# Kernel optimization log

Hardware: AMD Instinct MI355X
Metric: run time of the kernel (lower is better)

The kernel has to match this reference:

```python
import jax, jax.numpy as jnp
import numpy as np
import math


def _interp_linear(x, t_out):
    # x: [B, D, Lin] -> [B, D, t_out]; matches torch F.interpolate(mode='linear', align_corners=False)
    lin = x.shape[-1]
    pos = (jnp.arange(t_out, dtype=jnp.float32) + 0.5) * (lin / t_out) - 0.5
    pos = jnp.clip(pos, 0.0, lin - 1.0)
    lo = jnp.floor(pos).astype(jnp.int32)
    hi = jnp.minimum(lo + 1, lin - 1)
    w = pos - lo.astype(jnp.float32)
    return x[..., lo] * (1.0 - w) + x[..., hi] * w


def _forward(x, in_w, in_b, gq_w, gq_b, gk_w, gk_b, gv_w, gv_b, go_w, go_b, curv,
             wav0, wav1, wav2, wav3, wrec_w, wrec_b,
             te1_w, te1_b, te2_w, te2_b, td1_w, td1_b, td2_w, td2_b, bd_w, bd_b,
             cc_w, cc_b, ln_g, ln_b, mm1_w, mm1_b, mm2_w, mm2_b,
             dn1_w, dn1_b, dn2_w, dn2_b, dn3_w, dn3_b, out_w, out_b,
             noise_sched, noise):
    B, T, _ = x.shape
    L, H = curv.shape
    D = in_w.shape[1]
    hd = D // H
    dn = ('NCH', 'OIH', 'NCH')
    h = x @ in_w + in_b
    total_loss = jnp.float32(0.0)
    wavs = [wav0, wav1, wav2, wav3]
    for l in range(L):  # static small layer loop
        # ---- GeometricAttention (vectorized hyperbolic-distance softmax) ----
        q = (h @ gq_w[l] + gq_b[l]).reshape(B, T, H, hd)
        k = (h @ gk_w[l] + gk_b[l]).reshape(B, T, H, hd)
        v = (h @ gv_w[l] + gv_b[l]).reshape(B, T, H, hd)
        c = jnp.abs(curv[l]) + 1e-8                       # [H]
        cb = c[None, :, None, None]
        qn = jnp.einsum('bthd,bthd->bht', q, q)           # [B,H,T]
        kn = jnp.einsum('bthd,bthd->bht', k, k)
        qk = jnp.einsum('bihd,bjhd->bhij', q, k)          # [B,H,T,T]
        d2 = jnp.maximum(qn[:, :, :, None] + kn[:, :, None, :] - 2.0 * qk, 0.0)
        denom = jnp.maximum((1.0 - cb * qn[:, :, :, None]) * (1.0 - cb * kn[:, :, None, :]), 1e-5)
        arg = jnp.maximum(1.0 + cb * (2.0 * d2) / denom, 1.00001)
        dist = jnp.arccosh(arg) / jnp.sqrt(cb)
        attn = jax.nn.softmax(-dist, axis=-1)             # temperature = 1.0
        geom = jnp.einsum('bhij,bjhd->bihd', attn, v).reshape(B, T, D) @ go_w[l] + go_b[l]
        # ---- WaveletTransform ----
        xf = h.transpose(0, 2, 1)                          # [B,D,T]
        decomps = []
        for i, wv in enumerate(wavs):
            filt = jax.nn.softmax(wv[l], axis=-1)          # [D,K]
            K = filt.shape[-1]
            dec = jax.lax.conv_general_dilated(xf, filt[:, None, :], (1,), [(K - 1, 0)],
                                               feature_group_count=D, dimension_numbers=dn)
            dec = dec[:, :, ::2 ** (i + 1)]
            decomps.append(_interp_linear(dec, T))
        comb = jnp.concatenate(decomps, axis=1).transpose(0, 2, 1)  # [B,T,4D]
        wave = comb @ wrec_w[l] + wrec_b[l]
        # ---- TopologicalLayer ----
        tf = jax.nn.relu(h @ te1_w[l] + te1_b[l]) @ te2_w[l] + te2_b[l]
        topo = h + (jax.nn.relu(tf @ td1_w[l] + td1_b[l]) @ td2_w[l] + td2_b[l])
        bd = tf @ bd_w[l] + bd_b[l]
        total_loss = total_loss + jnp.mean(jax.nn.relu(bd[..., 0] - bd[..., 1] + 0.1))
        # ---- CausalConvolution (kernel 3, dilation 2**l) ----
        dil = 2 ** l
        pad = 2 * dil
        cc = jax.lax.conv_general_dilated(h.transpose(0, 2, 1), cc_w[l], (1,), [(pad, 0)],
                                          rhs_dilation=(dil,), dimension_numbers=dn)
        cc = (cc + cc_b[l][None, :, None]).transpose(0, 2, 1)
        # ---- combine + LayerNorm (dropout is identity in eval) ----
        s = geom + wave + topo + cc
        mu = jnp.mean(s, axis=-1, keepdims=True)
        var = jnp.var(s, axis=-1, keepdims=True)
        h = (s - mu) / jnp.sqrt(var + 1e-5) * ln_g + ln_b
    # ---- manifold mixer (T > 1 branch) ----
    last = h[:, -1]
    pen = h[:, -2]
    mix = jnp.tanh(jnp.concatenate([last, pen], axis=-1) @ mm1_w + mm1_b) @ mm2_w + mm2_b
    cur = last + mix
    # ---- diffusion refinement ----
    half = D // 2
    emb_f = jnp.exp(jnp.arange(half, dtype=jnp.float32) * (-math.log(10000.0) / (half - 1)))
    S = noise.shape[0]
    for t in range(S):  # static diffusion_steps=10
        noisy = cur + noise[t] * noise_sched[t]
        te = jnp.full((B, 1), float(t), dtype=jnp.float32) * emb_f[None, :]
        temb = jnp.concatenate([jnp.sin(te), jnp.cos(te)], axis=-1)  # [B,D]
        di = jnp.concatenate([noisy, temb], axis=-1)
        npred = jax.nn.silu(jax.nn.silu(di @ dn1_w + dn1_b) @ dn2_w + dn2_b) @ dn3_w + dn3_b
        cur = cur - npred * noise_sched[t]
    pred = cur @ out_w + out_b
    return pred, total_loss


def setup_inputs() -> dict:
    key = jax.random.key(0)
    B, T, Din, D, L, H, P, S = 16, 256, 384, 512, 6, 8, 64, 10
    ctr = [0]
    def rn(shape, s=0.05):
        ctr[0] += 1
        return jax.random.normal(jax.random.fold_in(key, ctr[0]), shape, jnp.float32) * s
    d = {}
    d['x'] = rn((B, T, Din), 1.0)
    d['in_w'] = rn((Din, D)); d['in_b'] = rn((D,), 0.01)
    for nm in ['gq', 'gk', 'gv', 'go']:
        d[nm + '_w'] = rn((L, D, D)); d[nm + '_b'] = rn((L, D), 0.01)
    d['curv'] = rn((L, H), 1.0)
    for i in range(4):
        d['wav%d' % i] = rn((L, D, 2 ** (i + 2)), 1.0)
    d['wrec_w'] = rn((L, 4 * D, D)); d['wrec_b'] = rn((L, D), 0.01)
    d['te1_w'] = rn((L, D, P)); d['te1_b'] = rn((L, P), 0.01)
    d['te2_w'] = rn((L, P, P)); d['te2_b'] = rn((L, P), 0.01)
    d['td1_w'] = rn((L, P, D)); d['td1_b'] = rn((L, D), 0.01)
    d['td2_w'] = rn((L, D, D)); d['td2_b'] = rn((L, D), 0.01)
    d['bd_w'] = rn((L, P, 2)); d['bd_b'] = rn((L, 2), 0.01)
    d['cc_w'] = rn((L, D, D, 3)); d['cc_b'] = rn((L, D), 0.01)
    d['ln_g'] = jnp.ones((D,), jnp.float32); d['ln_b'] = jnp.zeros((D,), jnp.float32)
    d['mm1_w'] = rn((2 * D, D)); d['mm1_b'] = rn((D,), 0.01)
    d['mm2_w'] = rn((D, D)); d['mm2_b'] = rn((D,), 0.01)
    d['dn1_w'] = rn((2 * D, D)); d['dn1_b'] = rn((D,), 0.01)
    d['dn2_w'] = rn((D, D)); d['dn2_b'] = rn((D,), 0.01)
    d['dn3_w'] = rn((D, D)); d['dn3_b'] = rn((D,), 0.01)
    d['out_w'] = rn((D, Din)); d['out_b'] = rn((Din,), 0.01)
    d['noise_sched'] = jnp.linspace(0.1, 0.9, S).astype(jnp.float32)
    d['noise'] = rn((S, B, D), 1.0)
    return d


def reference(x, in_w, in_b, gq_w, gq_b, gk_w, gk_b, gv_w, gv_b, go_w, go_b, curv,
              wav0, wav1, wav2, wav3, wrec_w, wrec_b,
              te1_w, te1_b, te2_w, te2_b, td1_w, td1_b, td2_w, td2_b, bd_w, bd_b,
              cc_w, cc_b, ln_g, ln_b, mm1_w, mm1_b, mm2_w, mm2_b,
              dn1_w, dn1_b, dn2_w, dn2_b, dn3_w, dn3_b, out_w, out_b,
              noise_sched, noise):
    return _forward(x, in_w, in_b, gq_w, gq_b, gk_w, gk_b, gv_w, gv_b, go_w, go_b, curv,
                    wav0, wav1, wav2, wav3, wrec_w, wrec_b,
                    te1_w, te1_b, te2_w, te2_b, td1_w, td1_b, td2_w, td2_b, bd_w, bd_b,
                    cc_w, cc_b, ln_g, ln_b, mm1_w, mm1_b, mm2_w, mm2_b,
                    dn1_w, dn1_b, dn2_w, dn2_b, dn3_w, dn3_b, out_w, out_b,
                    noise_sched, noise)
```

## Files before the change

### kernel.cpp

```cpp
#include <hip/hip_runtime.h>
#include <hip/hip_bf16.h>
#include <math.h>

#define BB 16
#define TT 256
#define DIN 384
#define DD 512
#define LL 6
#define HH 8
#define PP 64
#define SS 10
#define BT (BB*TT)

enum { ACT_NONE=0, ACT_RELU=1, ACT_TANH=2, ACT_SILU=3, ACT_RELU_TAIL=4 };

typedef __attribute__((ext_vector_type(8))) short bf16x8;
typedef __attribute__((ext_vector_type(4))) float f32x4;
typedef __hip_bfloat16 bh16;

typedef const __attribute__((address_space(1))) void gvoid_t;
typedef __attribute__((address_space(3))) void lvoid_t;
__device__ __forceinline__ void gload16(const void* g, void* l) {
    __builtin_amdgcn_global_load_lds((gvoid_t*)g, (lvoid_t*)l, 16, 0, 0);
}
// ... 412 lines not shown
                float dist = logf(arg + sqrtf((arg - 1.f) * (arg + 1.f))) * isc;
                float lg = -dist;
                acc[fm][fn][r] = lg;
                rmax[fm][r] = fmaxf(rmax[fm][r], lg);
            }
    #pragma unroll
    for (int off = 1; off < 16; off <<= 1)
        #pragma unroll
        for (int fm = 0; fm < 2; ++fm)
            #pragma unroll
            for (int r = 0; r < 4; ++r)
                rmax[fm][r] = fmaxf(rmax[fm][r], __shfl_xor(rmax[fm][r], off));
    if ((lane & 15) == 0)
        #pragma unroll
        for (int fm = 0; fm < 2; ++fm)
            #pragma unroll
            for (int r = 0; r < 4; ++r)
                redA[wn][wm*32 + fm*16 + (lane>>4)*4 + r] = rmax[fm][r];
    __syncthreads();
    #pragma unroll
    for (int fm = 0; fm < 2; ++fm)
        #pragma unroll
        for (int r = 0; r < 4; ++r)
            rmax[fm][r] = fmaxf(rmax[fm][r], redA[wn ^ 1][wm*32 + fm*16 + (lane>>4)*4 + r]);
    float rsum[2][4];
    #pragma unroll
    for (int fm = 0; fm < 2; ++fm)
        #pragma unroll
        for (int r = 0; r < 4; ++r) rsum[fm][r] = 0.f;
    #pragma unroll
    for (int fm = 0; fm < 2; ++fm)
        #pragma unroll
        for (int fn = 0; fn < 8; ++fn)
            #pragma unroll
            for (int r = 0; r < 4; ++r) {
                float e = expf(acc[fm][fn][r] - rmax[fm][r]);
                acc[fm][fn][r] = e;
                rsum[fm][r] += e;
            }
    #pragma unroll
    for (int off = 1; off < 16; off <<= 1)
        #pragma unroll
        for (int fm = 0; fm < 2; ++fm)
            #pragma unroll
            for (int r = 0; r < 4; ++r)
                rsum[fm][r] += __shfl_xor(rsum[fm][r], off);
    if ((lane & 15) == 0)
        #pragma unroll
        for (int fm = 0; fm < 2; ++fm)
            #pragma unroll
            for (int r = 0; r < 4; ++r)
                redB[wn][wm*32 + fm*16 + (lane>>4)*4 + r] = rsum[fm][r];
    __syncthreads();
    float pinv[2][4];
    #pragma unroll
    for (int fm = 0; fm < 2; ++fm)
        #pragma unroll
        for (int r = 0; r < 4; ++r)
            pinv[fm][r] = 1.f / (rsum[fm][r] + redB[wn ^ 1][wm*32 + fm*16 + (lane>>4)*4 + r]);

    f32x4 acc2[2][2];
    #pragma unroll
    for (int i = 0; i < 2; ++i)
        #pragma unroll
        for (int j = 0; j < 2; ++j) acc2[i][j] = (f32x4){0.f,0.f,0.f,0.f};

    const bh16* vbase = qkv + 1024 + hh * 64;
    for (int kt = 0; kt < 4; ++kt) {
        __syncthreads();
        if (wn == (kt >> 1)) {
            int fnb = (kt & 1) * 4;
            #pragma unroll
            for (int fm = 0; fm < 2; ++fm)
                #pragma unroll
                for (int fnl = 0; fnl < 4; ++fnl)
                    #pragma unroll
                    for (int r = 0; r < 4; ++r) {
                        int rowl = wm*32 + fm*16 + (lane>>4)*4 + r;
                        int kl = fnl*16 + (lane & 15);
                        float p = acc[fm][fnb + fnl][r] * pinv[fm][r];
                        Ps[(rowl*8 + ((kl >> 3) ^ (rowl & 7)))*8 + (kl & 7)] = __float2bfloat16(p);
                    }
        }
        #pragma unroll
        for (int j = 0; j < 2; ++j) {
            int c = threadIdx.x + j*256;
            int tr = c >> 3, chk = c & 7;
            bf16x8 v = *(const bf16x8*)(vbase + (size_t)(b*256 + kt*64 + tr)*1600 + chk*8);
            *(bf16x8*)(&Vst[tr*72 + chk*8]) = v;
        }
        __syncthreads();
        #pragma unroll
        for (int j = 0; j < 2; ++j) {
            int c = threadIdx.x + j*256;
            int col = c & 63, chk = c >> 6;
            bf16x8 v;
            #pragma unroll
            for (int e = 0; e < 8; ++e)
                v[e] = (short)Vst[(chk*8 + e)*72 + col];
            Bv[col*8 + (chk ^ (col & 7))] = v;
        }
        __syncthreads();

        bf16x8 pa[2][2], vb[2][2];
        #pragma unroll
        for (int fm = 0; fm < 2; ++fm) {
            int row = wm*32 + fm*16 + (lane & 15);
            #pragma unroll
            for (int ks = 0; ks < 2; ++ks)
                pa[fm][ks] = ((bf16x8*)Ps)[row*8 + ((ks*4 + (lane>>4)) ^ (row & 7))];
        }
        #pragma unroll
        for (int fn = 0; fn < 2; ++fn) {
            int col = wn*32 + fn*16 + (lane & 15);
            #pragma unroll
            for (int ks = 0; ks < 2; ++ks)
                vb[fn][ks] = Bv[col*8 + ((ks*4 + (lane>>4)) ^ (col & 7))];
        }
        #pragma unroll
        for (int ks = 0; ks < 2; ++ks)
            #pragma unroll
            for (int fm = 0; fm < 2; ++fm)
                #pragma unroll
                for (int fn = 0; fn < 2; ++fn)
                    acc2[fm][fn] = __builtin_amdgcn_mfma_f32_16x16x32_bf16(
                        pa[fm][ks], vb[fn][ks], acc2[fm][fn], 0, 0, 0);
    }

    #pragma unroll
    for (int fm = 0; fm < 2; ++fm)
        #pragma unroll
        for (int fn = 0; fn < 2; ++fn)
            #pragma unroll
            for (int r = 0; r < 4; ++r) {
                int rowl = wm*32 + fm*16 + (lane>>4)*4 + r;
                int col = wn*32 + fn*16 + (lane & 15);
                gmb[((size_t)(b*256 + rh*64 + rowl))*512 + hh*64 + col] =
                    __float2bfloat16(acc2[fm][fn][r]);
            }
}

__global__ __launch_bounds__(256) void fgemm_kernel(
    const bh16* __restrict__ A0, const bh16* __restrict__ A1,
    const bh16* __restrict__ A2, const bh16* __restrict__ A3,
    const bh16* __restrict__ B0, const bh16* __restrict__ B1,
    const bh16* __restrict__ B2, const bh16* __restrict__ B3,
    const float* __restrict__ bias,
    float* __restrict__ Cf0, float* __restrict__ Cf1,
    float* __restrict__ Cf2, float* __restrict__ Cf3,
    int dil, const bh16* __restrict__ zp)
{
    __shared__ bf16x8 As[128*8];
    __shared__ bf16x8 Bs[64*8];

    int bx = blockIdx.x, by = blockIdx.y;
    xcd_swizzle_always(bx, by);
    const int zz = blockIdx.z;
    const int ktlo = zz * 18;
    const int kthi = ktlo + 18;

    const int tid  = threadIdx.x;
    const int lane = tid & 63, w = tid >> 6;
    const int wm = w >> 1, wn = w & 1;
    const int row0 = by * 128, col0 = bx * 64;

    f32x4 acc[4][2];
    #pragma unroll
    for (int i = 0; i < 4; ++i)
        #pragma unroll
        for (int j = 0; j < 2; ++j) acc[i][j] = (f32x4){0.f,0.f,0.f,0.f};

    for (int kt = ktlo; kt < kthi; ++kt) {
        const bh16* Aseg; const bh16* Bseg;
        int ldas, ldbs, k0, mask_sh, addr_sh;
        if (kt < 8) {
            Aseg = A0; Bseg = B0; ldas = 512; ldbs = 512;
            k0 = kt << 6; mask_sh = 0; addr_sh = 0;
        } else if (kt < 40) {
            Aseg = A1; Bseg = B1; ldas = 2048; ldbs = 2048;
            k0 = (kt - 8) << 6; mask_sh = 0; addr_sh = 0;
        } else if (kt < 48) {
            Aseg = A2; Bseg = B2; ldas = 512; ldbs = 512;
            k0 = (kt - 40) << 6; mask_sh = 0; addr_sh = 0;
        } else {
            int kl = kt - 48, tap = kl >> 3;
            Aseg = A3; Bseg = B3; ldas = 512; ldbs = 1536;
            k0 = kl << 6;
            mask_sh = (2 - tap) * dil;
            addr_sh = mask_sh + tap;
        }
        #pragma unroll
        for (int j = 0; j < 4; ++j) {
            int c = ((w*4 + j) << 6) + lane;
            int row = c >> 3, chk = c & 7;
            int schk = chk ^ (row & 7);
            int grow = row0 + row;
            const bh16* src = ((grow & 255) >= mask_sh)
                ? (Aseg + (size_t)(grow - addr_sh)*ldas + k0 + schk*8) : zp;
            gload16(src, &As[(w*4 + j) * 64]);
        }
        #pragma unroll
        for (int j = 0; j < 2; ++j) {
            int c = ((w*2 + j) << 6) + lane;
            int row = c >> 3, chk = c & 7;
            int schk = chk ^ (row & 7);
            int gcol = col0 + row;
            gload16(Bseg + (size_t)gcol*ldbs + k0 + schk*8, &Bs[(w*2 + j) * 64]);
        }
        asm volatile("s_waitcnt vmcnt(0)" ::: "memory");
        __syncthreads();

        bf16x8 a[4][2], b[2][2];
        #pragma unroll
        for (int fm = 0; fm < 4; ++fm) {
            int row = wm*64 + fm*16 + (lane & 15);
            #pragma unroll
            for (int ks = 0; ks < 2; ++ks)
                a[fm][ks] = As[row*8 + ((ks*4 + (lane>>4)) ^ (row & 7))];
        }
        #pragma unroll
        for (int fn = 0; fn < 2; ++fn) {
            int col = wn*32 + fn*16 + (lane & 15);
            #pragma unroll
            for (int ks = 0; ks < 2; ++ks)
                b[fn][ks] = Bs[col*8 + ((ks*4 + (lane>>4)) ^ (col & 7))];
        }
        #pragma unroll
        for (int ks = 0; ks < 2; ++ks)
            #pragma unroll
            for (int fm = 0; fm < 4; ++fm)
                #pragma unroll
                for (int fn = 0; fn < 2; ++fn)
                    acc[fm][fn] = __builtin_amdgcn_mfma_f32_16x16x32_bf16(
                        a[fm][ks], b[fn][ks], acc[fm][fn], 0, 0, 0);
        __syncthreads();
    }

    float* Cf = (zz == 0) ? Cf0 : (zz == 1) ? Cf1 : (zz == 2) ? Cf2 : Cf3;
    #pragma unroll
    for (int fm = 0; fm < 4; ++fm) {
        #pragma unroll
        for (int fn = 0; fn < 2; ++fn) {
            int gc = col0 + wn*32 + fn*16 + (lane & 15);
            float bs = (zz == 0) ? bias[gc] : 0.f;
            #pragma unroll
            for (int r = 0; r < 4; ++r) {
                int gr = row0 + wm*64 + fm*16 + (lane>>4)*4 + r;
                Cf[(size_t)gr*512 + gc] = acc[fm][fn][r] + bs;
            }
        }
    }
}

__global__ __launch_bounds__(256) void hgemm16_kernel(
    const bh16* __restrict__ A, int lda, long aZ,
    const bh16* __restrict__ Bt, int ldb,
    const float* __restrict__ bias,
    const float* __restrict__ pre,
    float* __restrict__ Of, bh16* __restrict__ Ob, long oZ,
    int N, int K, int act,
    float* __restrict__ curf, bh16* __restrict__ curb,
    const float* __restrict__ scaleptr)
{
    const int z = blockIdx.z;
    A += (long)z * aZ;
    const int lane = threadIdx.x & 63, w = threadIdx.x >> 6;
    const int col0 = blockIdx.x * 64 + w * 16;
    const int ar = lane & 15;
    const int koff = (lane >> 4) * 8;
    const bh16* arow = A + (size_t)ar * lda + koff;
    const bh16* brow = Bt + (size_t)(col0 + ar) * ldb + koff;
    f32x4 acc = {0.f, 0.f, 0.f, 0.f};
    const int nkt = K >> 5;
    for (int kt0 = 0; kt0 < nkt; kt0 += 8) {
        bf16x8 av[8], bv[8];
        #pragma unroll
        for (int j = 0; j < 8; ++j) {
            av[j] = *(const bf16x8*)(arow + (size_t)(kt0 + j) * 32);
            bv[j] = *(const bf16x8*)(brow + (size_t)(kt0 + j) * 32);
        }
        #pragma unroll
        for (int j = 0; j < 8; ++j)
            acc = __builtin_amdgcn_mfma_f32_16x16x32_bf16(av[j], bv[j], acc, 0, 0, 0);
    }
    const int col = col0 + ar;
    float bs = bias ? bias[col] : 0.f;
    float sc = scaleptr ? *scaleptr : 0.f;
    #pragma unroll
    for (int r = 0; r < 4; ++r) {
        int row = (lane >> 4) * 4 + r;
        float v = acc[r] + bs;
        if (pre) v += pre[(size_t)row * N + col];
        if (act == ACT_SILU)      v = v / (1.f + expf(-v));
        else if (act == ACT_TANH) v = tanhf(v);
        if (curf) {
            size_t o = (size_t)row * 512 + col;
            float nc = curf[o] - v * sc;
            curf[o] = nc;
            curb[o] = __float2bfloat16(nc);
        } else {
            size_t o = (size_t)z * oZ + (size_t)row * N + col;
            if (Of) Of[o] = v;
            if (Ob) Ob[o] = __float2bfloat16(v);
        }
    }
}

__global__ __launch_bounds__(256) void wave4_kernel(const bh16* __restrict__ hb,
                                                    const float* __restrict__ wav0,
                                                    const float* __restrict__ wav1,
                                                    const float* __restrict__ wav2,
                                                    const float* __restrict__ wav3,
                                                    int l,
                                                    bh16* __restrict__ comb)
{
    __shared__ float dtile[66 * 64];
    __shared__ float ftile[32 * 64];
    const int dblk = blockIdx.x;
    const int iy = blockIdx.y;
    const int b = blockIdx.z;
    const int i = iy >> 1, thalf = iy & 1;
    const int Karr[4] = {4, 8, 16, 32};
    const int K = Karr[i], sv = 2 << i, Ti = 128 >> i;
    const int tid = threadIdx.x;
    const int dbase = dblk * 64;
    if (tid < 64) {
        const float* wsrc = (i == 0) ? wav0 : (i == 1) ? wav1 : (i == 2) ? wav2 : wav3;
        const float* row = wsrc + ((size_t)l * DD + dbase + tid) * K;
        float mx = -1e30f;
        for (int k = 0; k < K; ++k) mx = fmaxf(mx, row[k]);
        float s = 0.f;
        for (int k = 0; k < K; ++k) { float e = expf(row[k] - mx); ftile[k*64 + tid] = e; s += e; }
        float inv = 1.f / s;
        for (int k = 0; k < K; ++k) ftile[k*64 + tid] *= inv;
    }
    const float invsv = 1.f / (float)sv;
    const int t0 = thalf * 128;
    float p0 = ((float)t0 + 0.5f) * invsv - 0.5f;
    p0 = fminf(fmaxf(p0, 0.f), (float)(Ti - 1));
    const int jbase = (int)p0;
    float p1 = ((float)(t0 + 127) + 0.5f) * invsv - 0.5f;
    p1 = fminf(fmaxf(p1, 0.f), (float)(Ti - 1));
    const int him = min((int)p1 + 1, Ti - 1);
    const int jcount = him - jbase + 1;
    __syncthreads();
    const bh16* hcol = hb + (size_t)b * (TT * DD) + dbase;
    for (int e = tid; e < jcount * 64; e += 256) {
        int jl = e >> 6, d0 = e & 63;
        int j = jbase + jl;
        int tb = j * sv - (K - 1);
        float acc = 0.f;
        #pragma unroll 4
        for (int k = 0; k < K; ++k) {
            int t = tb + k;
            if (t >= 0)
                acc += b2f(*(const unsigned short*)(hcol + (size_t)t * DD + d0)) * ftile[k * 64 + d0];
        }
        dtile[jl * 64 + d0] = acc;
    }
    __syncthreads();
    for (int e = tid; e < 128 * 64; e += 256) {
        int tl = e >> 6, d0 = e & 63;
        int t = t0 + tl;
        float pos = ((float)t + 0.5f) * invsv - 0.5f;
        pos = fminf(fmaxf(pos, 0.f), (float)(Ti - 1));
        int lo = (int)pos;
        int hi = min(lo + 1, Ti - 1);
        float w = pos - (float)lo;
        float v = dtile[(lo - jbase) * 64 + d0] * (1.f - w) + dtile[(hi - jbase) * 64 + d0] * w;
        comb[((size_t)b * TT + t) * 2048 + i * 512 + dbase + d0] = __float2bfloat16(v);
    }
}

__global__ __launch_bounds__(256) void add_ln_kernel(const float* __restrict__ s0, const float* __restrict__ s1,
                                                     const float* __restrict__ s2, const float* __restrict__ s3,
                                                     float* __restrict__ h, bh16* __restrict__ hb,
                                                     const float* __restrict__ g, const float* __restrict__ be)
{
    int lane = threadIdx.x & 63, wid = threadIdx.x >> 6;
    size_t row = (size_t)blockIdx.x * 4 + wid;
    const float* sr0 = s0 + row * DD;
    const float* sr1 = s1 + row * DD;
    const float* sr2 = s2 + row * DD;
    const float* sr3 = s3 + row * DD;
    float* hr = h + row * DD;
    bh16* hbr = hb + row * DD;
    float xv[8]; float sum = 0.f;
    #pragma unroll
    for (int u = 0; u < 8; ++u) {
        int c = lane + u * 64;
        xv[u] = sr0[c] + sr1[c] + sr2[c] + sr3[c] + hr[c];
        sum += xv[u];
    }
    #pragma unroll
    for (int off = 32; off; off >>= 1) sum += __shfl_xor(sum, off);
    float mu = sum * (1.f / 512.f);
    float sq = 0.f;
    #pragma unroll
    for (int u = 0; u < 8; ++u) { float d = xv[u] - mu; sq += d * d; }
    #pragma unroll
    for (int off = 32; off; off >>= 1) sq += __shfl_xor(sq, off);
    float rstd = 1.f / sqrtf(sq * (1.f / 512.f) + 1e-5f);
    #pragma unroll
    for (int u = 0; u < 8; ++u) {
        int c = lane + u * 64;
        float v = (xv[u] - mu) * rstd * g[c] + be[c];
        hr[c] = v;
        hbr[c] = __float2bfloat16(v);
    }
}

__global__ __launch_bounds__(256) void wtrans_kernel(const float* __restrict__ W, bh16* __restrict__ Wt,
                                                     int K, int N, long lstride)
{
    int l = blockIdx.z;
    const float* Wl = W + (size_t)l * K * N;
    bh16* Wo = Wt + (size_t)l * lstride;
    __shared__ float tile[32][33];
    int n0 = blockIdx.x * 32, k0 = blockIdx.y * 32;
    int lx = threadIdx.x & 31, ly = threadIdx.x >> 5;
    #pragma unroll
    for (int j = 0; j < 4; ++j) {
        int kk = ly + j * 8;
        tile[kk][lx] = Wl[(size_t)(k0 + kk) * N + n0 + lx];
    }
    __syncthreads();
    #pragma unroll
    for (int j = 0; j < 4; ++j) {
        int nr = ly + j * 8;
        Wo[(size_t)(n0 + nr) * K + k0 + lx] = __float2bfloat16(tile[lx][nr]);
    }
}

__global__ __launch_bounds__(256) void wtrans4_kernel(const float* __restrict__ gq, const float* __restrict__ gk,
                                                      const float* __restrict__ gv, const float* __restrict__ te1,
                                                      bh16* __restrict__ qkvT)
{
    int bxx = blockIdx.x, l = blockIdx.z;
    const float* W; long off; int N; int n0;
    if (bxx < 16)      { W = gq;  off = 0;      N = 512; n0 = bxx * 32; }
    else if (bxx < 32) { W = gk;  off = 262144; N = 512; n0 = (bxx - 16) * 32; }
    else if (bxx < 48) { W = gv;  off = 524288; N = 512; n0 = (bxx - 32) * 32; }
    else               { W = te1; off = 786432; N = 64;  n0 = (bxx - 48) * 32; }
    const float* Wl = W + (size_t)l * 512 * N;
    bh16* Wo = qkvT + (size_t)l * 819200 + off;
    __shared__ float tile[32][33];
    int k0 = blockIdx.y * 32;
    int lx = threadIdx.x & 31, ly = threadIdx.x >> 5;
    #pragma unroll
    for (int j = 0; j < 4; ++j) {
        int kk = ly + j * 8;
        tile[kk][lx] = Wl[(size_t)(k0 + kk) * N + n0 + lx];
    }
    __syncthreads();
    #pragma unroll
    for (int j = 0; j < 4; ++j) {
        int nr = ly + j * 8;
        Wo[(size_t)(n0 + nr) * 512 + k0 + lx] = __float2bfloat16(tile[lx][nr]);
    }
}

__global__ __launch_bounds__(256) void ccconv_kernel(const float* __restrict__ ccw, bh16* __restrict__ ccT)
{
    size_t idx = (size_t)blockIdx.x * 256 + threadIdx.x;
    int i = idx & 511; size_t rem = idx >> 9;
    int tap = (int)(rem % 3); rem /= 3;
    int o = (int)(rem & 511); int l = (int)(rem >> 9);
    ccT[idx] = __float2bfloat16(ccw[(((size_t)l*512 + o)*512 + i)*3 + tap]);
}

__global__ __launch_bounds__(256) void qkvbias_kernel(const float* __restrict__ qb_, const float* __restrict__ kb_,
                                                      const float* __restrict__ vb_, const float* __restrict__ t1b_,
                                                      float* __restrict__ ob,
                                                      const float* __restrict__ gob, const float* __restrict__ wrb,
                                                      const float* __restrict__ tdb, const float* __restrict__ ccb,
                                                      float* __restrict__ bsum)
{
    int idx = blockIdx.x * 256 + threadIdx.x;
    if (idx < 6 * 1600) {
        int l = idx / 1600, n = idx % 1600;
        float v = (n < 512) ? qb_[l*512 + n]
                : (n < 1024) ? kb_[l*512 + n - 512]
                : (n < 1536) ? vb_[l*512 + n - 1024]
                : t1b_[l*64 + n - 1536];
        ob[idx] = v;
    }
    if (idx < 6 * 512) {
        bsum[idx] = gob[idx] + wrb[idx] + tdb[idx] + ccb[idx];
    }
}

__global__ __launch_bounds__(256) void convx_kernel(const float* __restrict__ x, bh16* __restrict__ xb)
{
    size_t idx = (size_t)blockIdx.x * 256 + threadIdx.x;
    xb[idx] = __float2bfloat16(x[idx]);
}

__global__ __launch_bounds__(256) void build_E_kernel(const float* __restrict__ noise, const float* __restrict__ sched,
                                                      bh16* __restrict__ E)
{
    int idx = blockIdx.x * 256 + threadIdx.x;
    if (idx >= SS * BB * 1024) return;
    int k = idx & 1023; int rem = idx >> 10; int b = rem & 15; int t = rem >> 4;
    float v;
    if (k < 512) {
        v = sched[t] * noise[((size_t)t * BB + b) * 512 + k];
    } else {
        int j = k - 512;
        const float kfac = -9.210340371976184f / 255.f;
        v = (j < 256) ? sinf((float)t * expf((float)j * kfac))
                      : cosf((float)t * expf((float)(j - 256) * kfac));
    }
    E[idx] = __float2bfloat16(v);
}

__global__ void init_kernel(bh16* zp, float* loss)
{
    int t = threadIdx.x;
    if (t < 64) zp[t] = __float2bfloat16(0.f);
    if (t == 64) *loss = 0.f;
}

__global__ __launch_bounds__(256) void build_cat16_kernel(const float* __restrict__ h, bh16* __restrict__ catb)
{
    int idx = blockIdx.x * 256 + threadIdx.x;
    if (idx >= BB * 1024) return;
    int k = idx & 1023, b = idx >> 10;
    float v = (k < 512) ? h[((size_t)b * TT + 255) * DD + k]
                        : h[((size_t)b * TT + 254) * DD + (k - 512)];
    catb[idx] = __float2bfloat16(v);
}

__global__ __launch_bounds__(256) void cur_init2_kernel(const float* __restrict__ h, const float* __restrict__ mix,
                                                        float* __restrict__ curf, bh16* __restrict__ curb)
{
    int idx = blockIdx.x * 256 + threadIdx.x;
    if (idx >= BB * DD) return;
    int c = idx & 511, b = idx >> 9;
    float v = h[((size_t)b * TT + 255) * DD + c] + mix[idx];
    curf[idx] = v;
    curb[idx] = __float2bfloat16(v);
}

__global__ void fail_kernel(float* p) { p[0] = 1e30f; }

extern "C" void kernel_launch(void* const* d_in, const int* in_sizes, int n_in,
                              void* d_out, int out_size, void* d_ws, size_t ws_size,
                              hipStream_t stream)
{
    const float* x      = (const float*)d_in[0];
    const float* in_w   = (const float*)d_in[1];
    const float* in_b   = (const float*)d_in[2];
    const float* gq_w   = (const float*)d_in[3];
    const float* gq_b   = (const float*)d_in[4];
    const float* gk_w   = (const float*)d_in[5];
    const float* gk_b   = (const float*)d_in[6];
    const float* gv_w   = (const float*)d_in[7];
    const float* gv_b   = (const float*)d_in[8];
    const float* go_w   = (const float*)d_in[9];
    const float* go_b   = (const float*)d_in[10];
    const float* curv   = (const float*)d_in[11];
    const float* wav0   = (const float*)d_in[12];
    const float* wav1   = (const float*)d_in[13];
    const float* wav2   = (const float*)d_in[14];
    const float* wav3   = (const float*)d_in[15];
    const float* wrec_w = (const float*)d_in[16];
    const float* wrec_b = (const float*)d_in[17];
    const float* te1_w  = (const float*)d_in[18];
    const float* te1_b  = (const float*)d_in[19];
    const float* te2_w  = (const float*)d_in[20];
    const float* te2_b  = (const float*)d_in[21];
    const float* td1_w  = (const float*)d_in[22];
    const float* td1_b  = (const float*)d_in[23];
    const float* td2_w  = (const float*)d_in[24];
    const float* td2_b  = (const float*)d_in[25];
    const float* bd_w   = (const float*)d_in[26];
    const float* bd_b   = (const float*)d_in[27];
    const float* cc_w   = (const float*)d_in[28];
    const float* cc_b   = (const float*)d_in[29];
    const float* ln_g   = (const float*)d_in[30];
    const float* ln_b   = (const float*)d_in[31];
    const float* mm1_w  = (const float*)d_in[32];
    const float* mm1_b  = (const float*)d_in[33];
    const float* mm2_w  = (const float*)d_in[34];
    const float* mm2_b  = (const float*)d_in[35];
    const float* dn1_w  = (const float*)d_in[36];
    const float* dn1_b  = (const float*)d_in[37];
    const float* dn2_w  = (const float*)d_in[38];
    const float* dn2_b  = (const float*)d_in[39];
    const float* dn3_w  = (const float*)d_in[40];
    const float* dn3_b  = (const float*)d_in[41];
    const float* out_w  = (const float*)d_in[42];
    const float* out_b  = (const float*)d_in[43];
    const float* nsched = (const float*)d_in[44];
    const float* noise  = (const float*)d_in[45];
    float* out = (float*)d_out;
    float* ws  = (float*)d_ws;

    const size_t o_h   = 0;
    const size_t o_dec = 2097152;
    const size_t o_s   = 4194304;
    const size_t o_tf  = 6291456;
    const size_t o_at  = 6619136;
    const size_t o_mix = 15038464;
    const size_t o_cur = 15046656;
    const size_t o_qkb = 15054848;
    const size_t o_bs  = 15064448;
    const size_t FP32_TOTAL = 15095808;
    const size_t b_xb   = 0;
    const size_t b_hb   = 1572864;
    const size_t b_qkv  = 3670016;
    const size_t b_pb   = 12320768;
    const size_t b_gmb  = 20709376;
    const size_t b_tdb  = 22806528;
    const size_t b_zp   = 25165824;
    const size_t b_inwT = 25166336;
    const size_t b_qkvT = 25362944;
    const size_t b_goT  = 30278144;
    const size_t b_wrT  = 31851008;
    const size_t b_td1T = 38142464;
    const size_t b_td2T = 38339072;
    const size_t b_te2T = 39911936;
    const size_t b_ccT  = 39936512;
    const size_t BF16_TOTAL = 44655104;
    const size_t TOTAL_BYTES = FP32_TOTAL * 4 + BF16_TOTAL * 2;
    if (ws_size < TOTAL_BYTES) { fail_kernel<<<1, 1, 0, stream>>>(out); return; }

    float* h_   = ws + o_h;
    float* s2_  = ws + o_dec;
    float* s_   = ws + o_s;
    float* at_  = ws + o_at;
    float* s3_  = at_ + 4194304;
    float* s4_  = at_ + 6291456;
    float* mixb = ws + o_mix;
    float* curf = ws + o_cur;
    float* qkvbias = ws + o_qkb;
    float* bsum = ws + o_bs;
    bh16* bp   = (bh16*)(ws + FP32_TOTAL);
    bh16* xb   = bp + b_xb;
    bh16* hb   = bp + b_hb;
    bh16* qkvb = bp + b_qkv;
    bh16* pb   = bp + b_pb;
    bh16* gmb  = bp + b_gmb;
    bh16* tdb  = bp + b_tdb;
    bh16* zp   = bp + b_zp;
    bh16* inwT = bp + b_inwT;
    bh16* qkvT = bp + b_qkvT;
    bh16* goT  = bp + b_goT;
    bh16* wrT  = bp + b_wrT;
    bh16* td1T = bp + b_td1T;
    bh16* td2T = bp + b_td2T;
    bh16* te2T = bp + b_te2T;
    bh16* ccT  = bp + b_ccT;
    bh16* combb = (bh16*)at_;

    bh16* dn1T  = pb;
    bh16* dn2T  = pb + 524288;
    bh16* dn3T  = pb + 786432;
    bh16* mm1T  = pb + 1048576;
    bh16* mm2T  = pb + 1572864;
    bh16* outT  = pb + 1835008;
    bh16* E16   = pb + 2031616;
    bh16* cat16 = pb + 2195456;
    bh16* tmb16 = pb + 2211840;
    bh16* cur16 = pb + 2220032;
    bh16* d1b16 = pb + 2228224;
    bh16* d2b16 = pb + 2236416;
    float* pre1 = s2_;

    auto mgp = [&](const bh16* A, int lda, const bh16* Bt, int ldb,
                   const float* bias, float* Cf, bh16* Cb, int ldc,
                   int M, int N, int K, int shift, int accum, int act) {
        dim3 g((N + 63) / 64, M / 128, 1);
        mgemm_kernel<<<g, 256, 0, stream>>>(A, lda, Bt, ldb, bias, Cf, Cb, ldc, N, K,
                                            shift, accum, act, zp);
    };
    auto hg = [&](const bh16* A, int lda, long aZ, const bh16* Bt, int ldb,
                  const float* bias, const float* pre, float* Of, bh16* Ob, long oZ,
                  int N, int K, int act, float* cf, bh16* cb, const float* sp, int nz) {
        hgemm16_kernel<<<dim3(N / 64, 1, nz), 256, 0, stream>>>(
            A, lda, aZ, Bt, ldb, bias, pre, Of, Ob, oZ, N, K, act, cf, cb, sp);
    };

    init_kernel<<<1, 128, 0, stream>>>(zp, out + BB * DIN);
    convx_kernel<<<BT * DIN / 256, 256, 0, stream>>>(x, xb);
    wtrans_kernel<<<dim3(DD/32, DIN/32, 1), 256, 0, stream>>>(in_w, inwT, DIN, DD, (long)DIN*DD);
    wtrans4_kernel<<<dim3(50, 16, 6), 256, 0, stream>>>(gq_w, gk_w, gv_w, te1_w, qkvT);
    qkvbias_kernel<<<38, 256, 0, stream>>>(gq_b, gk_b, gv_b, te1_b, qkvbias,
                                           go_b, wrec_b, td2_b, cc_b, bsum);
    wtrans_kernel<<<dim3(16, 16, 6), 256, 0, stream>>>(go_w, goT, DD, DD, (long)DD*DD);
    wtrans_kernel<<<dim3(16, 64, 6), 256, 0, stream>>>(wrec_w, wrT, 2048, DD, 2048L*DD);
    wtrans_kernel<<<dim3(16, 2, 6), 256, 0, stream>>>(td1_w, td1T, PP, DD, (long)PP*DD);
    wtrans_kernel<<<dim3(16, 16, 6), 256, 0, stream>>>(td2_w, td2T, DD, DD, (long)DD*DD);
    wtrans_kernel<<<dim3(2, 2, 6), 256, 0, stream>>>(te2_w, te2T, PP, PP, (long)PP*PP);
    ccconv_kernel<<<18432, 256, 0, stream>>>(cc_w, ccT);

    mgp(xb, DIN, inwT, DIN, in_b, h_, hb, DD, BT, DD, DIN, 0, 0, ACT_NONE);

    for (int l = 0; l < LL; ++l) {
        mgp(hb, DD, qkvT + (size_t)l*819200, DD, qkvbias + (size_t)l*1600,
            nullptr, qkvb, 1600, BT, 1600, DD, 0, 0, ACT_RELU_TAIL);
        fattn_kernel<<<dim3(4, 128), 256, 0, stream>>>(qkvb, curv + (size_t)l*HH, gmb);
        wave4_kernel<<<dim3(8, 8, 16), 256, 0, stream>>>(hb, wav0, wav1, wav2, wav3, l, combb);
        topo_kernel<<<dim3(8, 32), 256, 0, stream>>>(
            qkvb + 1536, te2T + (size_t)l*4096, te2_b + (size_t)l*PP,
            td1T + (size_t)l*32768, td1_b + (size_t)l*DD,
            bd_w + (size_t)l*PP*2, bd_b + (size_t)l*2, out + BB*DIN, tdb);
        fgemm_kernel<<<dim3(8, 32, 4), 256, 0, stream>>>(
            gmb, combb, tdb, hb,
            goT + (size_t)l*262144, wrT + (size_t)l*1048576,
            td2T + (size_t)l*262144, ccT + (size_t)l*786432,
            bsum + (size_t)l*512, s_, s2_, s3_, s4_, 1 << l, zp);
        add_ln_kernel<<<BT/4, 256, 0, stream>>>(s_, s2_, s3_, s4_, h_, hb, ln_g, ln_b);
    }

    wtrans_kernel<<<dim3(16, 32, 1), 256, 0, stream>>>(dn1_w, dn1T, 1024, 512, 0L);
    wtrans_kernel<<<dim3(16, 16, 1), 256, 0, stream>>>(dn2_w, dn2T, 512, 512, 0L);
    wtrans_kernel<<<dim3(16, 16, 1), 256, 0, stream>>>(dn3_w, dn3T, 512, 512, 0L);
    wtrans_kernel<<<dim3(16, 32, 1), 256, 0, stream>>>(mm1_w, mm1T, 1024, 512, 0L);
    wtrans_kernel<<<dim3(16, 16, 1), 256, 0, stream>>>(mm2_w, mm2T, 512, 512, 0L);
    wtrans_kernel<<<dim3(12, 16, 1), 256, 0, stream>>>(out_w, outT, 512, 384, 0L);
    build_E_kernel<<<640, 256, 0, stream>>>(noise, nsched, E16);
    hg(E16, 1024, 16*1024, dn1T, 1024, dn1_b, nullptr, pre1, nullptr, 8192,
       512, 1024, ACT_NONE, nullptr, nullptr, nullptr, SS);
    build_cat16_kernel<<<64, 256, 0, stream>>>(h_, cat16);
    hg(cat16, 1024, 0, mm1T, 1024, mm1_b, nullptr, nullptr, tmb16, 0,
       512, 1024, ACT_TANH, nullptr, nullptr, nullptr, 1);
    hg(tmb16, 512, 0, mm2T, 512, mm2_b, nullptr, mixb, nullptr, 0,
       512, 512, ACT_NONE, nullptr, nullptr, nullptr, 1);
    cur_init2_kernel<<<32, 256, 0, stream>>>(h_, mixb, curf, cur16);
    for (int t = 0; t < SS; ++t) {
        hg(cur16, 512, 0, dn1T, 1024, nullptr, pre1 + (size_t)t*8192, nullptr, d1b16, 0,
           512, 512, ACT_SILU, nullptr, nullptr, nullptr, 1);
        hg(d1b16, 512, 0, dn2T, 512, dn2_b, nullptr, nullptr, d2b16, 0,
           512, 512, ACT_SILU, nullptr, nullptr, nullptr, 1);
        hg(d2b16, 512, 0, dn3T, 512, dn3_b, nullptr, nullptr, nullptr, 0,
           512, 512, ACT_NONE, curf, cur16, nsched + t, 1);
    }
    hg(cur16, 512, 0, outT, 512, out_b, nullptr, out, nullptr, 0,
       384, 512, ACT_NONE, nullptr, nullptr, nullptr, 1);
}
```

Before: 1.015 ms.

## Fuse diffusion head GEMM chain into one persistent kernel with grid barriers

Replaces the roughly 35 small head GEMM launches (mix MLP, 10 denoise steps of three GEMMs, output projection) with a single 8-block persistent kernel. Blocks sync between stages through an atomic-counter grid barrier, and the cat/cur init kernels are folded into it. The six head weight transposes are also merged into one launch. This removes launch overhead and tail gaps on a latency-bound serial chain. The cost is spin-wait barriers, reliance on all 8 blocks being co-resident, and only 8 CUs doing the work.

```diff
diff --git a/kernel.cpp b/kernel.cpp
--- a/kernel.cpp
+++ b/kernel.cpp
@@ -738,6 +738,145 @@
             size_t o = (size_t)z * oZ + (size_t)row * N + col;
             if (Of) Of[o] = v;
             if (Ob) Ob[o] = __float2bfloat16(v);
+        }
+    }
+}
+
+__device__ __forceinline__ f32x4 hslice(const bh16* A, int lda, const bh16* Bt, int ldb,
+                                        int col0, int K, int lane)
+{
+    const int ar = lane & 15;
+    const int koff = (lane >> 4) * 8;
+    const bh16* arow = A + (size_t)ar * lda + koff;
+    const bh16* brow = Bt + (size_t)(col0 + ar) * ldb + koff;
+    f32x4 acc = {0.f, 0.f, 0.f, 0.f};
+    const int nkt = K >> 5;
+    for (int kt0 = 0; kt0 < nkt; kt0 += 8) {
+        bf16x8 av[8], bv[8];
+        #pragma unroll
+        for (int j = 0; j < 8; ++j) {
+            av[j] = *(const bf16x8*)(arow + (size_t)(kt0 + j) * 32);
+            bv[j] = *(const bf16x8*)(brow + (size_t)(kt0 + j) * 32);
+        }
+        #pragma unroll
+        for (int j = 0; j < 8; ++j)
+            acc = __builtin_amdgcn_mfma_f32_16x16x32_bf16(av[j], bv[j], acc, 0, 0, 0);
+    }
+    return acc;
+}
+
+__device__ __forceinline__ void headbar(int* ctr, int* bar)
+{
+    __threadfence();
+    __syncthreads();
+    if (threadIdx.x == 0) {
+        __hip_atomic_fetch_add(ctr, 1, __ATOMIC_ACQ_REL, __HIP_MEMORY_SCOPE_AGENT);
+        *bar += 8;
+        while (__hip_atomic_load(ctr, __ATOMIC_ACQUIRE, __HIP_MEMORY_SCOPE_AGENT) < *bar)
+            __builtin_amdgcn_s_sleep(8);
+    }
+    __syncthreads();
+    __threadfence();
+}
+
+__global__ __launch_bounds__(256) void head_kernel(
+    const float* __restrict__ h,
+    const bh16* __restrict__ mm1T, const float* __restrict__ mm1b,
+    const bh16* __restrict__ mm2T, const float* __restrict__ mm2b,
+    const bh16* __restrict__ dn1T,
+    const bh16* __restrict__ dn2T, const float* __restrict__ dn2b,
+    const bh16* __restrict__ dn3T, const float* __restrict__ dn3b,
+    const bh16* __restrict__ outT, const float* __restrict__ outb,
+    const float* __restrict__ pre1, const float* __restrict__ nsched,
+    bh16* __restrict__ tmb16, float* __restrict__ curf, bh16* __restrict__ cur16,
+    bh16* __restrict__ d1b16, bh16* __restrict__ d2b16,
+    float* __restrict__ out, int* __restrict__ ctr)
+{
+    __shared__ __align__(16) bh16 catL[16 * 1032];
+    const int bx = blockIdx.x;
+    const int tid = threadIdx.x;
+    const int lane = tid & 63, w = tid >> 6;
+    int bar = 0;
+
+    for (int e = tid; e < 16 * 1024; e += 256) {
+        int k = e & 1023, b = e >> 10;
+        float v = (k < 512) ? h[((size_t)b * TT + 255) * DD + k]
+                            : h[((size_t)b * TT + 254) * DD + (k - 512)];
+        catL[b * 1032 + k] = __float2bfloat16(v);
+    }
+    __syncthreads();
+
+    const int col0 = bx * 64 + w * 16;
+    const int colr = col0 + (lane & 15);
+
+    {
+        f32x4 acc = hslice((const bh16*)catL, 1032, mm1T, 1024, col0, 1024, lane);
+        float bs = mm1b[colr];
+        #pragma unroll
+        for (int r = 0; r < 4; ++r) {
+            int row = (lane >> 4) * 4 + r;
+            tmb16[(size_t)row * 512 + colr] = __float2bfloat16(tanhf(acc[r] + bs));
+        }
+    }
+    headbar(ctr, &bar);
+    {
+        f32x4 acc = hslice(tmb16, 512, mm2T, 512, col0, 512, lane);
+        float bs = mm2b[colr];
+        #pragma unroll
+        for (int r = 0; r < 4; ++r) {
+            int row = (lane >> 4) * 4 + r;
+            float cv = h[((size_t)row * TT + 255) * DD + colr] + acc[r] + bs;
+            curf[(size_t)row * 512 + colr] = cv;
+            cur16[(size_t)row * 512 + colr] = __float2bfloat16(cv);
+        }
+    }
+    headbar(ctr, &bar);
+    for (int t = 0; t < SS; ++t) {
+        float sc = nsched[t];
+        {
+            f32x4 acc = hslice(cur16, 512, dn1T, 1024, col0, 512, lane);
+            #pragma unroll
+            for (int r = 0; r < 4; ++r) {
+                int row = (lane >> 4) * 4 + r;
+                float v = acc[r] + pre1[(size_t)t * 8192 + row * 512 + colr];
+                v = v / (1.f + expf(-v));
+                d1b16[(size_t)row * 512 + colr] = __float2bfloat16(v);
+            }
+        }
+        headbar(ctr, &bar);
+        {
+            f32x4 acc = hslice(d1b16, 512, dn2T, 512, col0, 512, lane);
+            float bs = dn2b[colr];
+            #pragma unroll
+            for (int r = 0; r < 4; ++r) {
+                int row = (lane >> 4) * 4 + r;
+                float v = acc[r] + bs;
+                v = v / (1.f + expf(-v));
+                d2b16[(size_t)row * 512 + colr] = __float2bfloat16(v);
+            }
+        }
+        headbar(ctr, &bar);
+        {
+            f32x4 acc = hslice(d2b16, 512, dn3T, 512, col0, 512, lane);
+            float bs = dn3b[colr];
+            #pragma unroll
+            for (int r = 0; r < 4; ++r) {
+                int row = (lane >> 4) * 4 + r;
+                size_t o = (size_t)row * 512 + colr;
+                float nc = curf[o] - (acc[r] + bs) * sc;
+                curf[o] = nc;
+                cur16[o] = __float2bfloat16(nc);
+            }
+        }
+        headbar(ctr, &bar);
+    }
+    if (bx < 6) {
+        f32x4 acc = hslice(cur16, 512, outT, 512, col0, 512, lane);
+        float bs = outb[colr];
+        #pragma unroll
+        for (int r = 0; r < 4; ++r) {
+            int row = (lane >> 4) * 4 + r;
+            out[(size_t)row * 384 + colr] = acc[r] + bs;
         }
     }
 }
@@ -896,6 +1035,38 @@
     }
 }
 
+__global__ __launch_bounds__(256) void wtransH_kernel(
+    const float* __restrict__ mm1w, const float* __restrict__ mm2w,
+    const float* __restrict__ dn1w, const float* __restrict__ dn2w,
+    const float* __restrict__ dn3w, const float* __restrict__ outw,
+    bh16* __restrict__ mm1T, bh16* __restrict__ mm2T, bh16* __restrict__ dn1T,
+    bh16* __restrict__ dn2T, bh16* __restrict__ dn3T, bh16* __restrict__ outT)
+{
+    int bx = blockIdx.x;
+    const float* W; bh16* Wo; int K, N, bloc;
+    if (bx < 512)       { W = mm1w; Wo = mm1T; K = 1024; N = 512; bloc = bx; }
+    else if (bx < 768)  { W = mm2w; Wo = mm2T; K = 512;  N = 512; bloc = bx - 512; }
+    else if (bx < 1280) { W = dn1w; Wo = dn1T; K = 1024; N = 512; bloc = bx - 768; }
+    else if (bx < 1536) { W = dn2w; Wo = dn2T; K = 512;  N = 512; bloc = bx - 1280; }
+    else if (bx < 1792) { W = dn3w; Wo = dn3T; K = 512;  N = 512; bloc = bx - 1536; }
+    else                { W = outw; Wo = outT; K = 512;  N = 384; bloc = bx - 1792; }
+    int nblk = N / 32;
+    int n0 = (bloc % nblk) * 32, k0 = (bloc / nblk) * 32;
+    __shared__ float tile[32][33];
+    int lx = threadIdx.x & 31, ly = threadIdx.x >> 5;
+    #pragma unroll
+    for (int j = 0; j < 4; ++j) {
+        int kk = ly + j * 8;
+        tile[kk][lx] = W[(size_t)(k0 + kk) * N + n0 + lx];
+    }
+    __syncthreads();
+    #pragma unroll
+    for (int j = 0; j < 4; ++j) {
+        int nr = ly + j * 8;
+        Wo[(size_t)(n0 + nr) * K + k0 + lx] = __float2bfloat16(tile[lx][nr]);
+    }
+}
+
 __global__ __launch_bounds__(256) void ccconv_kernel(const float* __restrict__ ccw, bh16* __restrict__ ccT)
 {
     size_t idx = (size_t)blockIdx.x * 256 + threadIdx.x;
@@ -950,32 +1121,12 @@
     E[idx] = __float2bfloat16(v);
 }
 
-__global__ void init_kernel(bh16* zp, float* loss)
+__global__ void init_kernel(bh16* zp, float* loss, int* ctr)
 {
     int t = threadIdx.x;
     if (t < 64) zp[t] = __float2bfloat16(0.f);
     if (t == 64) *loss = 0.f;
-}
-
-__global__ __launch_bounds__(256) void build_cat16_kernel(const float* __restrict__ h, bh16* __restrict__ catb)
-{
-    int idx = blockIdx.x * 256 + threadIdx.x;
-    if (idx >= BB * 1024) return;
-    int k = idx & 1023, b = idx >> 10;
-    float v = (k < 512) ? h[((size_t)b * TT + 255) * DD + k]
-                        : h[((size_t)b * TT + 254) * DD + (k - 512)];
-    catb[idx] = __float2bfloat16(v);
-}
-
-__global__ __launch_bounds__(256) void cur_init2_kernel(const float* __restrict__ h, const float* __restrict__ mix,
-                                                        float* __restrict__ curf, bh16* __restrict__ curb)
-{
-    int idx = blockIdx.x * 256 + threadIdx.x;
-    if (idx >= BB * DD) return;
-    int c = idx & 511, b = idx >> 9;
-    float v = h[((size_t)b * TT + 255) * DD + c] + mix[idx];
-    curf[idx] = v;
-    curb[idx] = __float2bfloat16(v);
+    if (t == 65) *ctr = 0;
 }
 
 __global__ void fail_kernel(float* p) { p[0] = 1e30f; }
@@ -1036,12 +1187,12 @@
     const size_t o_h   = 0;
     const size_t o_dec = 2097152;
     const size_t o_s   = 4194304;
-    const size_t o_tf  = 6291456;
     const size_t o_at  = 6619136;
     const size_t o_mix = 15038464;
     const size_t o_cur = 15046656;
     const size_t o_qkb = 15054848;
     const size_t o_bs  = 15064448;
+    const size_t o_ctr = 15067520;
     const size_t FP32_TOTAL = 15095808;
     const size_t b_xb   = 0;
     const size_t b_hb   = 1572864;
@@ -1068,10 +1219,10 @@
     float* at_  = ws + o_at;
     float* s3_  = at_ + 4194304;
     float* s4_  = at_ + 6291456;
-    float* mixb = ws + o_mix;
     float* curf = ws + o_cur;
     float* qkvbias = ws + o_qkb;
     float* bsum = ws + o_bs;
+    int*   ctr  = (int*)(ws + o_ctr);
     bh16* bp   = (bh16*)(ws + FP32_TOTAL);
     bh16* xb   = bp + b_xb;
     bh16* hb   = bp + b_hb;
@@ -1097,7 +1248,6 @@
     bh16* mm2T  = pb + 1572864;
     bh16* outT  = pb + 1835008;
     bh16* E16   = pb + 2031616;
-    bh16* cat16 = pb + 2195456;
     bh16* tmb16 = pb + 2211840;
     bh16* cur16 = pb + 2220032;
     bh16* d1b16 = pb + 2228224;
@@ -1111,14 +1261,8 @@
         mgemm_kernel<<<g, 256, 0, stream>>>(A, lda, Bt, ldb, bias, Cf, Cb, ldc, N, K,
                                             shift, accum, act, zp);
     };
-    auto hg = [&](const bh16* A, int lda, long aZ, const bh16* Bt, int ldb,
-                  const float* bias, const float* pre, float* Of, bh16* Ob, long oZ,
-                  int N, int K, int act, float* cf, bh16* cb, const float* sp, int nz) {
-        hgemm16_kernel<<<dim3(N / 64, 1, nz), 256, 0, stream>>>(
-            A, lda, aZ, Bt, ldb, bias, pre, Of, Ob, oZ, N, K, act, cf, cb, sp);
-    };
-
-    init_kernel<<<1, 128, 0, stream>>>(zp, out + BB * DIN);
+
+    init_kernel<<<1, 128, 0, stream>>>(zp, out + BB * DIN, ctr);
     convx_kernel<<<BT * DIN / 256, 256, 0, stream>>>(x, xb);
     wtrans_kernel<<<dim3(DD/32, DIN/32, 1), 256, 0, stream>>>(in_w, inwT, DIN, DD, (long)DIN*DD);
     wtrans4_kernel<<<dim3(50, 16, 6), 256, 0, stream>>>(gq_w, gk_w, gv_w, te1_w, qkvT);
@@ -1150,29 +1294,13 @@
         add_ln_kernel<<<BT/4, 256, 0, stream>>>(s_, s2_, s3_, s4_, h_, hb, ln_g, ln_b);
     }
 
-    wtrans_kernel<<<dim3(16, 32, 1), 256, 0, stream>>>(dn1_w, dn1T, 1024, 512, 0L);
-    wtrans_kernel<<<dim3(16, 16, 1), 256, 0, stream>>>(dn2_w, dn2T, 512, 512, 0L);
-    wtrans_kernel<<<dim3(16, 16, 1), 256, 0, stream>>>(dn3_w, dn3T, 512, 512, 0L);
-    wtrans_kernel<<<dim3(16, 32, 1), 256, 0, stream>>>(mm1_w, mm1T, 1024, 512, 0L);
-    wtrans_kernel<<<dim3(16, 16, 1), 256, 0, stream>>>(mm2_w, mm2T, 512, 512, 0L);
-    wtrans_kernel<<<dim3(12, 16, 1), 256, 0, stream>>>(out_w, outT, 512, 384, 0L);
+    wtransH_kernel<<<1984, 256, 0, stream>>>(mm1_w, mm2_w, dn1_w, dn2_w, dn3_w, out_w,
+                                             mm1T, mm2T, dn1T, dn2T, dn3T, outT);
     build_E_kernel<<<640, 256, 0, stream>>>(noise, nsched, E16);
-    hg(E16, 1024, 16*1024, dn1T, 1024, dn1_b, nullptr, pre1, nullptr, 8192,
-       512, 1024, ACT_NONE, nullptr, nullptr, nullptr, SS);
-    build_cat16_kernel<<<64, 256, 0, stream>>>(h_, cat16);
-    hg(cat16, 1024, 0, mm1T, 1024, mm1_b, nullptr, nullptr, tmb16, 0,
-       512, 1024, ACT_TANH, nullptr, nullptr, nullptr, 1);
-    hg(tmb16, 512, 0, mm2T, 512, mm2_b, nullptr, mixb, nullptr, 0,
-       512, 512, ACT_NONE, nullptr, nullptr, nullptr, 1);
-    cur_init2_kernel<<<32, 256, 0, stream>>>(h_, mixb, curf, cur16);
-    for (int t = 0; t < SS; ++t) {
-        hg(cur16, 512, 0, dn1T, 1024, nullptr, pre1 + (size_t)t*8192, nullptr, d1b16, 0,
-           512, 512, ACT_SILU, nullptr, nullptr, nullptr, 1);
-        hg(d1b16, 512, 0, dn2T, 512, dn2_b, nullptr, nullptr, d2b16, 0,
-           512, 512, ACT_SILU, nullptr, nullptr, nullptr, 1);
-        hg(d2b16, 512, 0, dn3T, 512, dn3_b, nullptr, nullptr, nullptr, 0,
-           512, 512, ACT_NONE, curf, cur16, nsched + t, 1);
-    }
-    hg(cur16, 512, 0, outT, 512, out_b, nullptr, out, nullptr, 0,
-       384, 512, ACT_NONE, nullptr, nullptr, nullptr, 1);
-}
+    hgemm16_kernel<<<dim3(8, 1, SS), 256, 0, stream>>>(
+        E16, 1024, 16*1024, dn1T, 1024, dn1_b, nullptr, pre1, nullptr, 8192,
+        512, 1024, ACT_NONE, nullptr, nullptr, nullptr);
+    head_kernel<<<8, 256, 0, stream>>>(
+        h_, mm1T, mm1_b, mm2T, mm2_b, dn1T, dn2T, dn2_b, dn3T, dn3_b,
+        outT, out_b, pre1, nsched, tmb16, curf, cur16, d1b16, d2b16, out, ctr);
+}
```

Measured after the change: 1.003 ms. No clear change (-1.2%).
